# Kernel optimization log

Measured on AMD Instinct MI355X. Metric: run time of the kernel, lower is better.

## Reference

```python
import jax, jax.numpy as jnp
import numpy as np

N = 50000
EPS = 1e-12


def sage_conv(x, src, dst, Wl, bl, Wr):
    # mean aggregation of source features into target nodes
    msg = x[src]                                            # [E, d]
    agg = jax.ops.segment_sum(msg, dst, num_segments=N)     # [N, d]
    cnt = jax.ops.segment_sum(jnp.ones_like(src, dtype=x.dtype), dst, num_segments=N)
    agg = agg / jnp.maximum(cnt, 1.0)[:, None]
    out = agg @ Wl + bl + x @ Wr                            # lin_l(aggr) + lin_r(x)
    # L2 normalize (PyG normalize=True)
    nrm = jnp.maximum(jnp.linalg.norm(out, axis=-1, keepdims=True), EPS)
    return out / nrm


def setup_inputs() -> dict:
    key = jax.random.key(0)
    ks = jax.random.split(key, 12)
    d_in, d_h, d_out = 128, 128, 40
    E = 800000
    x = jax.random.normal(ks[0], (N, d_in), dtype=jnp.float32)
    edge_index = jax.random.randint(ks[1], (2, E), 0, N, dtype=jnp.int64)

    def xavier(k, shp):
        lim = np.sqrt(6.0 / (shp[0] + shp[1]))
        return jax.random.uniform(k, shp, jnp.float32, -lim, lim)

    return {
        "x": x, "edge_index": edge_index,
        "W1l": xavier(ks[2], (d_in, d_h)), "b1": jnp.zeros((d_h,), jnp.float32), "W1r": xavier(ks[3], (d_in, d_h)),
        "W2l": xavier(ks[4], (d_h, d_h)),  "b2": jnp.zeros((d_h,), jnp.float32), "W2r": xavier(ks[5], (d_h, d_h)),
        "W3l": xavier(ks[6], (d_h, d_h)),  "b3": jnp.zeros((d_h,), jnp.float32), "W3r": xavier(ks[7], (d_h, d_h)),
        "Wfc": xavier(ks[8], (d_h, d_out)), "bfc": jnp.zeros((d_out,), jnp.float32),
    }


def reference(x, edge_index, W1l, b1, W1r, W2l, b2, W2r, W3l, b3, W3r, Wfc, bfc):
    src, dst = edge_index[0], edge_index[1]
    h = sage_conv(x, src, dst, W1l, b1, W1r)
    h = jax.nn.relu(h)                       # dropout = identity at eval
    h = sage_conv(h, src, dst, W2l, b2, W2r)
    h = jax.nn.relu(h)
    h = sage_conv(h, src, dst, W3l, b3, W3r)
    return jax.nn.softmax(h @ Wfc + bfc, axis=-1)
```

## Files before the change

kernel.cpp:

```cpp
#include <hip/hip_runtime.h>
#include <math.h>

#define NN 50000
#define D 128
#define NBUK 256
#define EPB 4096

typedef __attribute__((ext_vector_type(8))) short bf16x8;
typedef __attribute__((ext_vector_type(4))) float f32x4;
typedef __attribute__((ext_vector_type(2))) float f32x2;

__device__ __forceinline__ float bf2f(unsigned short u) {
    union { unsigned int i; float f; } c;
    c.i = ((unsigned int)u) << 16;
    return c.f;
}
__device__ __forceinline__ unsigned short f2bf(float f) {
    union { float f; unsigned int i; } c;
    c.f = f;
    unsigned int u = c.i;
    return (unsigned short)((u + 0x7FFFu + ((u >> 16) & 1u)) >> 16);
}
__device__ __forceinline__ unsigned char f2f8(float v) {
    return (unsigned char)(__builtin_amdgcn_cvt_pk_fp8_f32(v, v, 0, false) & 0xFF);
}


__global__ __launch_bounds__(256) void cvtpack_kernel(const float* __restrict__ x,
                                                      unsigned short* __restrict__ xb,
                                                      unsigned int* __restrict__ x8,
                                                      int n4,
                                                      const float* __restrict__ W0,
                                                      const float* __restrict__ W1,
                                                      const float* __restrict__ W2,
                                                      const float* __restrict__ W3,
                                                      const float* __restrict__ W4,
                                                      const float* __restrict__ W5,
                                                      unsigned short* __restrict__ P,
                                                      const float* __restrict__ Wfc,
                                                      unsigned short* __restrict__ Pfc) {
    if (blockIdx.x < 384) {
        int i = blockIdx.x * 256 + threadIdx.x;
        int w = i >> 14, j = i & 16383;
        const float* W = (w == 0) ? W0 : (w == 1) ? W1 : (w == 2) ? W2
                       : (w == 3) ? W3 : (w == 4) ? W4 : W5;
        int e = j & 7, l = (j >> 3) & 63, n = (j >> 9) & 7, ks = j >> 12;
        int k = ks * 32 + (l >> 4) * 8 + e;
        int col = n * 16 + (l & 15);
        P[i] = f2bf(W[k * D + col]);
    } else if (blockIdx.x < 408) {
        int i = (blockIdx.x - 384) * 256 + threadIdx.x;
        int e = i & 7, l = (i >> 3) & 63, f = i >> 9;
        int ks = f / 3, n = f - ks * 3;
        int k = ks * 32 + (l >> 4) * 8 + e;
        int col = n * 16 + (l & 15);
        Pfc[i] = (col < 40) ? f2bf(Wfc[k * 40 + col]) : (unsigned short)0;
    } else {
        int i = (blockIdx.x - 408) * 256 + threadIdx.x;
        if (i < n4) {
            float4 v = ((const float4*)x)[i];
            ushort4 o;
            o.x = f2bf(v.x); o.y = f2bf(v.y); o.z = f2bf(v.z); o.w = f2bf(v.w);
            ((ushort4*)xb)[i] = o;
            unsigned int p01 = __builtin_amdgcn_cvt_pk_fp8_f32(v.x, v.y, 0, false);
            unsigned int p23 = __builtin_amdgcn_cvt_pk_fp8_f32(v.z, v.w, 0, false);
            x8[i] = (p01 & 0xFFFFu) | (p23 << 16);
        }
    }
}


__global__ __launch_bounds__(256) void bucket_hist_kernel(const int* __restrict__ e, int E,
                                                          int* __restrict__ bukcnt) {
    __shared__ int h[NBUK];
    int t = threadIdx.x;
    h[t] = 0;
    __syncthreads();
    int base = blockIdx.x * EPB;
    #pragma unroll
    for (int k = 0; k < 4; ++k) {
        int idx = base + k * 1024 + t * 4;
        if (idx + 4 <= E) {
            int4 d = *(const int4*)(e + E + idx);
            atomicAdd(&h[d.x >> 8], 1);
            atomicAdd(&h[d.y >> 8], 1);
            atomicAdd(&h[d.z >> 8], 1);
            atomicAdd(&h[d.w >> 8], 1);
        } else {
            for (int i = idx; i < E; ++i) atomicAdd(&h[e[E + i] >> 8], 1);
        }
    }
    __syncthreads();
    if (h[t]) atomicAdd(&bukcnt[t], h[t]);
}

__global__ __launch_bounds__(256) void bucket_scan_kernel(const int* __restrict__ bukcnt,
                                                          int* __restrict__ bukbase,
                                                          int* __restrict__ bukfill, int E) {
    __shared__ int wsum[4], woff[4];
    int t = threadIdx.x;
    int lane = t & 63, wave = t >> 6;
    int v = bukcnt[t];
    int incl = v;
    for (int off = 1; off < 64; off <<= 1) {
        int u = __shfl_up(incl, off);
        if (lane >= off) incl += u;
    }
    if (lane == 63) wsum[wave] = incl;
    __syncthreads();
    if (t == 0) {
        int r = 0;
        #pragma unroll
        for (int w = 0; w < 4; ++w) { woff[w] = r; r += wsum[w]; }
    }
    __syncthreads();
    int excl = woff[wave] + incl - v;
    bukbase[t] = excl;
    bukfill[t] = excl;
    if (t == 255) bukbase[NBUK] = E;
}

__global__ __launch_bounds__(256) void bucket_scatter_kernel(const int* __restrict__ e, int E,
                                                             int* __restrict__ bukfill,
                                                             unsigned int* __restrict__ ebuk) {
    __shared__ int h[NBUK];
    __shared__ int res[NBUK];
    int t = threadIdx.x;
    h[t] = 0;
    __syncthreads();
    int base = blockIdx.x * EPB;
    int4 d[4];
    #pragma unroll
    for (int k = 0; k < 4; ++k) {
        int idx = base + k * 1024 + t * 4;
        if (idx + 4 <= E) {
            d[k] = *(const int4*)(e + E + idx);
        } else {
            d[k].x = (idx + 0 < E) ? e[E + idx + 0] : -1;
            d[k].y = (idx + 1 < E) ? e[E + idx + 1] : -1;
            d[k].z = (idx + 2 < E) ? e[E + idx + 2] : -1;
            d[k].w = (idx + 3 < E) ? e[E + idx + 3] : -1;
        }
        if (d[k].x >= 0) atomicAdd(&h[d[k].x >> 8], 1);
        if (d[k].y >= 0) atomicAdd(&h[d[k].y >> 8], 1);
        if (d[k].z >= 0) atomicAdd(&h[d[k].z >> 8], 1);
        if (d[k].w >= 0) atomicAdd(&h[d[k].w >> 8], 1);
    }
    __syncthreads();
    res[t] = h[t] ? atomicAdd(&bukfill[t], h[t]) : 0;
    h[t] = 0;
    __syncthreads();
    #pragma unroll
    for (int k = 0; k < 4; ++k) {
        int idx = base + k * 1024 + t * 4;
        int4 s;
        if (idx + 4 <= E) {
            s = *(const int4*)(e + idx);
        } else {
            s.x = (idx + 0 < E) ? e[idx + 0] : 0;
            s.y = (idx + 1 < E) ? e[idx + 1] : 0;
            s.z = (idx + 2 < E) ? e[idx + 2] : 0;
            s.w = (idx + 3 < E) ? e[idx + 3] : 0;
        }
        if (d[k].x >= 0) { int b = d[k].x >> 8; int r = atomicAdd(&h[b], 1);
            ebuk[res[b] + r] = (unsigned int)(s.x & 0xFFFF) | ((unsigned int)(d[k].x & 255) << 16); }
        if (d[k].y >= 0) { int b = d[k].y >> 8; int r = atomicAdd(&h[b], 1);
            ebuk[res[b] + r] = (unsigned int)(s.y & 0xFFFF) | ((unsigned int)(d[k].y & 255) << 16); }
        if (d[k].z >= 0) { int b = d[k].z >> 8; int r = atomicAdd(&h[b], 1);
            ebuk[res[b] + r] = (unsigned int)(s.z & 0xFFFF) | ((unsigned int)(d[k].z & 255) << 16); }
        if (d[k].w >= 0) { int b = d[k].w >> 8; int r = atomicAdd(&h[b], 1);
            ebuk[res[b] + r] = (unsigned int)(s.w & 0xFFFF) | ((unsigned int)(d[k].w & 255) << 16); }
    }
}


__global__ __launch_bounds__(256) void cnt_scan_kernel(const unsigned int* __restrict__ ebuk,
                                                       const int* __restrict__ bukbase,
                                                       int* __restrict__ row_ptr,
                                                       float* __restrict__ inv_cnt,
                                                       int N, int E) {
    __shared__ int c[NBUK];
    __shared__ int wsum[4], woff[4];
    int t = threadIdx.x, b = blockIdx.x;
    c[t] = 0;
    __syncthreads();
    int lo = bukbase[b], hi = bukbase[b + 1];
    for (int i = lo + t; i < hi; i += 256) atomicAdd(&c[ebuk[i] >> 16], 1);
    __syncthreads();
    int v = c[t];
    int lane = t & 63, wave = t >> 6;
    int incl = v;
    for (int off = 1; off < 64; off <<= 1) {
        int u = __shfl_up(incl, off);
        if (lane >= off) incl += u;
    }
    if (lane == 63) wsum[wave] = incl;
    __syncthreads();
    if (t == 0) {
        int r = 0;
        #pragma unroll
        for (int w = 0; w < 4; ++w) { woff[w] = r; r += wsum[w]; }
    }
    __syncthreads();
    int excl = woff[wave] + incl - v;
    int g = b * NBUK + t;
    if (g < N) {
        row_ptr[g] = bukbase[b] + excl;
        inv_cnt[g] = 1.0f / fmaxf((float)v, 1.0f);
    }
    if (g == N) row_ptr[N] = E;
}

__global__ __launch_bounds__(256) void csr_scatter_kernel(const unsigned int* __restrict__ ebuk,
                                                          const int* __restrict__ bukbase,
                                                          const int* __restrict__ row_ptr,
                                                          unsigned short* __restrict__ csr_src,
                                                          int N) {
    __shared__ int rp[NBUK];
    __shared__ int lf[NBUK];
    int t = threadIdx.x, b = blockIdx.x;
    int g = b * NBUK + t;
    rp[t] = (g < N) ? row_ptr[g] : 0;
    lf[t] = 0;
    __syncthreads();
    int lo = bukbase[b], hi = bukbase[b + 1];
    for (int i = lo + t; i < hi; i += 256) {
        unsigned int v = ebuk[i];
        int dl = v >> 16;
        int r = atomicAdd(&lf[dl], 1);
        csr_src[rp[dl] + r] = (unsigned short)(v & 0xFFFF);
    }
}


__device__ __forceinline__ void acc_f8(float& x, float& y, float& z, float& w,
                                       unsigned int v) {
    f32x2 lo = __builtin_amdgcn_cvt_pk_f32_fp8(v, false);
    f32x2 hi = __builtin_amdgcn_cvt_pk_f32_fp8(v, true);
    x += lo.x; y += lo.y; z += hi.x; w += hi.y;
}

__global__ __launch_bounds__(256) void aggregate_kernel(const unsigned int* __restrict__ h8,
                                                        const int* __restrict__ row_ptr,
                                                        const unsigned short* __restrict__ csr_src,
                                                        const float* __restrict__ inv_cnt,
                                                        unsigned short* __restrict__ agg, int N) {
    int node = (int)((blockIdx.x * blockDim.x + threadIdx.x) >> 5);
    int l = threadIdx.x & 31;
    if (node >= N) return;
    int beg = row_ptr[node], end = row_ptr[node + 1];
    float a0x = 0.f, a0y = 0.f, a0z = 0.f, a0w = 0.f;
    float a1x = 0.f, a1y = 0.f, a1z = 0.f, a1w = 0.f;
    for (int base = beg; base < end; base += 32) {
        int idx = 0;
        if (base + l < end) idx = csr_src[base + l];
        int n = min(32, end - base);
        int j = 0;
        for (; j + 8 <= n; j += 8) {
            int s0 = __shfl(idx, j + 0, 32);
            int s1 = __shfl(idx, j + 1, 32);
            int s2 = __shfl(idx, j + 2, 32);
            int s3 = __shfl(idx, j + 3, 32);
            int s4 = __shfl(idx, j + 4, 32);
            int s5 = __shfl(idx, j + 5, 32);
            int s6 = __shfl(idx, j + 6, 32);
            int s7 = __shfl(idx, j + 7, 32);
            unsigned int v0 = h8[(size_t)s0 * 32 + l];
            unsigned int v1 = h8[(size_t)s1 * 32 + l];
            unsigned int v2 = h8[(size_t)s2 * 32 + l];
            unsigned int v3 = h8[(size_t)s3 * 32 + l];
            unsigned int v4 = h8[(size_t)s4 * 32 + l];
            unsigned int v5 = h8[(size_t)s5 * 32 + l];
            unsigned int v6 = h8[(size_t)s6 * 32 + l];
            unsigned int v7 = h8[(size_t)s7 * 32 + l];
            acc_f8(a0x, a0y, a0z, a0w, v0);
            acc_f8(a1x, a1y, a1z, a1w, v1);
            acc_f8(a0x, a0y, a0z, a0w, v2);
            acc_f8(a1x, a1y, a1z, a1w, v3);
            acc_f8(a0x, a0y, a0z, a0w, v4);
            acc_f8(a1x, a1y, a1z, a1w, v5);
            acc_f8(a0x, a0y, a0z, a0w, v6);
            acc_f8(a1x, a1y, a1z, a1w, v7);
        }
        for (; j < n; ++j) {
            int s = __shfl(idx, j, 32);
            acc_f8(a0x, a0y, a0z, a0w, h8[(size_t)s * 32 + l]);
        }
    }
    float iv = inv_cnt[node];
    ushort4 o;
    o.x = f2bf((a0x + a1x) * iv);
    o.y = f2bf((a0y + a1y) * iv);
    o.z = f2bf((a0z + a1z) * iv);
    o.w = f2bf((a0w + a1w) * iv);
    ((ushort4*)agg)[(size_t)node * 32 + l] = o;
}


__global__ __launch_bounds__(256) void sage_mfma_kernel(const unsigned short* __restrict__ aggb,
                                                        const unsigned short* __restrict__ xb,
                                                        const unsigned short* __restrict__ wlp,
                                                        const unsigned short* __restrict__ wrp,
                                                        const float* __restrict__ bl,
                                                        unsigned short* __restrict__ outb,
                                                        unsigned char* __restrict__ out8,
                                                        int N) {
    int t = threadIdx.x;
    int w = t >> 6;
    int l = t & 63;
    int rlo = l & 15;
    int khi = l >> 4;
    int row0 = blockIdx.x * 64 + w * 16;
    int rowA = row0 + rlo;
    bool okA = rowA < N;

    f32x4 acc[8];
    #pragma unroll
    for (int n = 0; n < 8; ++n) {
        float b = bl[n * 16 + rlo];
        acc[n] = (f32x4){b, b, b, b};
    }

    const short* Ap = (const short*)aggb + (size_t)(okA ? rowA : 0) * D + khi * 8;
    const short* Xp = (const short*)xb   + (size_t)(okA ? rowA : 0) * D + khi * 8;
    const short* WL = (const short*)wlp + l * 8;
    const short* WR = (const short*)wrp + l * 8;
    const bf16x8 Z = {0, 0, 0, 0, 0, 0, 0, 0};

    #pragma unroll 1
    for (int ks = 0; ks < 4; ++ks) {
        bf16x8 a = okA ? *(const bf16x8*)(Ap + ks * 32) : Z;
        #pragma unroll
        for (int n = 0; n < 8; ++n) {
            bf16x8 b = *(const bf16x8*)(WL + (ks * 8 + n) * 512);
            acc[n] = __builtin_amdgcn_mfma_f32_16x16x32_bf16(a, b, acc[n], 0, 0, 0);
        }
    }
    #pragma unroll 1
    for (int ks = 0; ks < 4; ++ks) {
        bf16x8 a = okA ? *(const bf16x8*)(Xp + ks * 32) : Z;
        #pragma unroll
        for (int n = 0; n < 8; ++n) {
            bf16x8 b = *(const bf16x8*)(WR + (ks * 8 + n) * 512);
            acc[n] = __builtin_amdgcn_mfma_f32_16x16x32_bf16(a, b, acc[n], 0, 0, 0);
        }
    }

    #pragma unroll
    for (int r = 0; r < 4; ++r) {
        float s = 0.f;
        #pragma unroll
        for (int n = 0; n < 8; ++n) s += acc[n][r] * acc[n][r];
        s += __shfl_xor(s, 1);
        s += __shfl_xor(s, 2);
        s += __shfl_xor(s, 4);
        s += __shfl_xor(s, 8);
        float inv = 1.0f / fmaxf(sqrtf(s), 1e-12f);
        int gr = row0 + khi * 4 + r;
        if (gr < N) {
            #pragma unroll
            for (int n = 0; n < 8; ++n) {
                float v = fmaxf(acc[n][r] * inv, 0.f);
                outb[(size_t)gr * D + n * 16 + rlo] = f2bf(v);
                out8[(size_t)gr * D + n * 16 + rlo] = f2f8(v);
            }
        }
    }
}


#define SH_STRIDE 136

__global__ __launch_bounds__(256) void sage_mfma_fc_kernel(const unsigned short* __restrict__ aggb,
                                                           const unsigned short* __restrict__ xb,
                                                           const unsigned short* __restrict__ wlp,
                                                           const unsigned short* __restrict__ wrp,
                                                           const float* __restrict__ bl,
                                                           const unsigned short* __restrict__ wfcp,
                                                           const float* __restrict__ bfc,
                                                           float* __restrict__ out, int N) {
    __shared__ unsigned short sH[64 * SH_STRIDE];
    int t = threadIdx.x;
    int w = t >> 6;
    int l = t & 63;
    int rlo = l & 15;
    int khi = l >> 4;
    int row0 = blockIdx.x * 64 + w * 16;
    int rowA = row0 + rlo;
    bool okA = rowA < N;

    f32x4 acc[8];
    #pragma unroll
    for (int n = 0; n < 8; ++n) {
        float b = bl[n * 16 + rlo];
        acc[n] = (f32x4){b, b, b, b};
    }

    const short* Ap = (const short*)aggb + (size_t)(okA ? rowA : 0) * D + khi * 8;
    const short* Xp = (const short*)xb   + (size_t)(okA ? rowA : 0) * D + khi * 8;
    const short* WL = (const short*)wlp + l * 8;
    const short* WR = (const short*)wrp + l * 8;
    const bf16x8 Z = {0, 0, 0, 0, 0, 0, 0, 0};

    #pragma unroll 1
    for (int ks = 0; ks < 4; ++ks) {
        bf16x8 a = okA ? *(const bf16x8*)(Ap + ks * 32) : Z;
        #pragma unroll
        for (int n = 0; n < 8; ++n) {
            bf16x8 b = *(const bf16x8*)(WL + (ks * 8 + n) * 512);
            acc[n] = __builtin_amdgcn_mfma_f32_16x16x32_bf16(a, b, acc[n], 0, 0, 0);
        }
    }
    #pragma unroll 1
    for (int ks = 0; ks < 4; ++ks) {
        bf16x8 a = okA ? *(const bf16x8*)(Xp + ks * 32) : Z;
        #pragma unroll
        for (int n = 0; n < 8; ++n) {
            bf16x8 b = *(const bf16x8*)(WR + (ks * 8 + n) * 512);
            acc[n] = __builtin_amdgcn_mfma_f32_16x16x32_bf16(a, b, acc[n], 0, 0, 0);
        }
    }

    #pragma unroll
    for (int r = 0; r < 4; ++r) {
        float s = 0.f;
        #pragma unroll
        for (int n = 0; n < 8; ++n) s += acc[n][r] * acc[n][r];
        s += __shfl_xor(s, 1);
        s += __shfl_xor(s, 2);
        s += __shfl_xor(s, 4);
        s += __shfl_xor(s, 8);
        float inv = 1.0f / fmaxf(sqrtf(s), 1e-12f);
        int lr = w * 16 + khi * 4 + r;
        #pragma unroll
        for (int n = 0; n < 8; ++n)
            sH[lr * SH_STRIDE + n * 16 + rlo] = f2bf(acc[n][r] * inv);
    }

    f32x4 fa[3];
    #pragma unroll
    for (int n = 0; n < 3; ++n) {
        int col = n * 16 + rlo;
        float b = (col < 40) ? bfc[col] : 0.f;
        fa[n] = (f32x4){b, b, b, b};
    }
    const short* WF = (const short*)wfcp + l * 8;
    const unsigned short* hrow = sH + (w * 16 + rlo) * SH_STRIDE + khi * 8;
    #pragma unroll
    for (int ks = 0; ks < 4; ++ks) {
        bf16x8 a = *(const bf16x8*)(hrow + ks * 32);
        #pragma unroll
        for (int n = 0; n < 3; ++n) {
            bf16x8 b = *(const bf16x8*)(WF + (ks * 3 + n) * 512);
            fa[n] = __builtin_amdgcn_mfma_f32_16x16x32_bf16(a, b, fa[n], 0, 0, 0);
        }
    }

    bool v2 = (rlo < 8);
    #pragma unroll
    for (int r = 0; r < 4; ++r) {
        float m = fmaxf(fa[0][r], fa[1][r]);
        if (v2) m = fmaxf(m, fa[2][r]);
        m = fmaxf(m, __shfl_xor(m, 1));
        m = fmaxf(m, __shfl_xor(m, 2));
        m = fmaxf(m, __shfl_xor(m, 4));
        m = fmaxf(m, __shfl_xor(m, 8));
        float e0 = expf(fa[0][r] - m);
        float e1 = expf(fa[1][r] - m);
        float e2 = v2 ? expf(fa[2][r] - m) : 0.f;
        float s = e0 + e1 + e2;
        s += __shfl_xor(s, 1);
        s += __shfl_xor(s, 2);
        s += __shfl_xor(s, 4);
        s += __shfl_xor(s, 8);
        float inv = 1.0f / s;
        int gr = row0 + khi * 4 + r;
        if (gr < N) {
            out[(size_t)gr * 40 + rlo]      = e0 * inv;
            out[(size_t)gr * 40 + 16 + rlo] = e1 * inv;
            if (v2) out[(size_t)gr * 40 + 32 + rlo] = e2 * inv;
        }
    }
}


extern "C" void kernel_launch(void* const* d_in, const int* in_sizes, int n_in,
                              void* d_out, int out_size, void* d_ws, size_t ws_size,
                              hipStream_t stream) {
    const float* x   = (const float*)d_in[0];
    const int*   e   = (const int*)d_in[1];
    const float* W1l = (const float*)d_in[2];
    const float* b1  = (const float*)d_in[3];
    const float* W1r = (const float*)d_in[4];
    const float* W2l = (const float*)d_in[5];
    const float* b2  = (const float*)d_in[6];
    const float* W2r = (const float*)d_in[7];
    const float* W3l = (const float*)d_in[8];
    const float* b3  = (const float*)d_in[9];
    const float* W3r = (const float*)d_in[10];
    const float* Wfc = (const float*)d_in[11];
    const float* bfc = (const float*)d_in[12];
    float* out = (float*)d_out;

    const int N = NN;
    const int E = in_sizes[1] / 2;

    unsigned char* p = (unsigned char*)d_ws;
    unsigned short* xb   = (unsigned short*)p; p += (size_t)N * D * 2;
    unsigned short* h1b  = (unsigned short*)p; p += (size_t)N * D * 2;
    unsigned short* h2b  = (unsigned short*)p; p += (size_t)N * D * 2;
    unsigned short* aggb = (unsigned short*)p; p += (size_t)N * D * 2;
    unsigned char*  xf8  = (unsigned char*)p;  p += (size_t)N * D;
    unsigned char*  h1f8 = (unsigned char*)p;  p += (size_t)N * D;
    unsigned short* wpk  = (unsigned short*)p; p += 6 * 16384 * 2;
    unsigned short* wfcp = (unsigned short*)p; p += 6144 * 2;
    float* inv_cnt = (float*)p; p += (size_t)N * 4;
    int* row_ptr = (int*)p; p += (size_t)(N + 4) * 4;
    int* bukcnt  = (int*)p; p += NBUK * 4;
    int* bukbase = (int*)p; p += (NBUK + 4) * 4;
    int* bukfill = (int*)p; p += NBUK * 4;
    unsigned int* ebuk = (unsigned int*)p; p += (size_t)E * 4;
    unsigned short* csr_src = (unsigned short*)p;
    unsigned char* h2f8 = xf8;

    unsigned short* w1lp = wpk;
    unsigned short* w1rp = wpk + 16384;
    unsigned short* w2lp = wpk + 2 * 16384;
    unsigned short* w2rp = wpk + 3 * 16384;
    unsigned short* w3lp = wpk + 4 * 16384;
    unsigned short* w3rp = wpk + 5 * 16384;

    hipMemsetAsync(bukcnt, 0, sizeof(int) * NBUK, stream);

    int n4 = N * D / 4;
    cvtpack_kernel<<<408 + (n4 + 255) / 256, 256, 0, stream>>>(
        x, xb, (unsigned int*)xf8, n4, W1l, W1r, W2l, W2r, W3l, W3r, wpk, Wfc, wfcp);

    int EB = (E + EPB - 1) / EPB;
    bucket_hist_kernel<<<EB, 256, 0, stream>>>(e, E, bukcnt);
    bucket_scan_kernel<<<1, 256, 0, stream>>>(bukcnt, bukbase, bukfill, E);
    bucket_scatter_kernel<<<EB, 256, 0, stream>>>(e, E, bukfill, ebuk);
    cnt_scan_kernel<<<NBUK, 256, 0, stream>>>(ebuk, bukbase, row_ptr, inv_cnt, N, E);
    csr_scatter_kernel<<<NBUK, 256, 0, stream>>>(ebuk, bukbase, row_ptr, csr_src, N);

    int aggBlocks = (N * 32 + 255) / 256;
    int sageBlocks = (N + 63) / 64;

    aggregate_kernel<<<aggBlocks, 256, 0, stream>>>((const unsigned int*)xf8, row_ptr,
                                                    csr_src, inv_cnt, aggb, N);
    sage_mfma_kernel<<<sageBlocks, 256, 0, stream>>>(aggb, xb, w1lp, w1rp, b1,
                                                     h1b, h1f8, N);

    aggregate_kernel<<<aggBlocks, 256, 0, stream>>>((const unsigned int*)h1f8, row_ptr,
                                                    csr_src, inv_cnt, aggb, N);
    sage_mfma_kernel<<<sageBlocks, 256, 0, stream>>>(aggb, h1b, w2lp, w2rp, b2,
                                                     h2b, h2f8, N);

    aggregate_kernel<<<aggBlocks, 256, 0, stream>>>((const unsigned int*)h2f8, row_ptr,
                                                    csr_src, inv_cnt, aggb, N);
    sage_mfma_fc_kernel<<<sageBlocks, 256, 0, stream>>>(aggb, h2b, w3lp, w3rp, b3,
                                                        wfcp, bfc, out, N);
}
```

Measured before the change: 172.4 us.

## Fuse neighbor aggregation into SAGE MFMA kernels and merge CSR build steps

Each layer's mean-aggregation gather now runs inside the MFMA kernel. It writes the 64 aggregated rows of a block into LDS instead of a global bf16 buffer, which removes the agg write and re-read and three kernel launches. The count-scan and CSR scatter kernels are merged into one, and the bucket-counter memset moves into the conversion kernel. The trade-off is that the gather loses its separate high-occupancy launch: 8 half-wave groups per block each handle 8 nodes before the MFMA phase can start, so latency hiding during the gather may suffer.

```diff
diff --git a/kernel.cpp b/kernel.cpp
--- a/kernel.cpp
+++ b/kernel.cpp
@@ -5,6 +5,7 @@
 #define D 128
 #define NBUK 256
 #define EPB 4096
+#define SH_STRIDE 136
 
 typedef __attribute__((ext_vector_type(8))) short bf16x8;
 typedef __attribute__((ext_vector_type(4))) float f32x4;
@@ -38,7 +39,8 @@
                                                       const float* __restrict__ W5,
                                                       unsigned short* __restrict__ P,
                                                       const float* __restrict__ Wfc,
-                                                      unsigned short* __restrict__ Pfc) {
+                                                      unsigned short* __restrict__ Pfc,
+                                                      int* __restrict__ bukcnt) {
     if (blockIdx.x < 384) {
         int i = blockIdx.x * 256 + threadIdx.x;
         int w = i >> 14, j = i & 16383;
@@ -49,6 +51,7 @@
         int col = n * 16 + (l & 15);
         P[i] = f2bf(W[k * D + col]);
     } else if (blockIdx.x < 408) {
+        if (blockIdx.x == 384) bukcnt[threadIdx.x] = 0;
         int i = (blockIdx.x - 384) * 256 + threadIdx.x;
         int e = i & 7, l = (i >> 3) & 63, f = i >> 9;
         int ks = f / 3, n = f - ks * 3;
@@ -174,12 +177,14 @@
 }
 
 
-__global__ __launch_bounds__(256) void cnt_scan_kernel(const unsigned int* __restrict__ ebuk,
-                                                       const int* __restrict__ bukbase,
-                                                       int* __restrict__ row_ptr,
-                                                       float* __restrict__ inv_cnt,
-                                                       int N, int E) {
+__global__ __launch_bounds__(256) void cnt_scan_scatter_kernel(const unsigned int* __restrict__ ebuk,
+                                                               const int* __restrict__ bukbase,
+                                                               int* __restrict__ row_ptr,
+                                                               float* __restrict__ inv_cnt,
+                                                               unsigned short* __restrict__ csr_src,
+                                                               int N, int E) {
     __shared__ int c[NBUK];
+    __shared__ int rp[NBUK];
     __shared__ int wsum[4], woff[4];
     int t = threadIdx.x, b = blockIdx.x;
     c[t] = 0;
@@ -203,32 +208,20 @@
     }
     __syncthreads();
     int excl = woff[wave] + incl - v;
+    rp[t] = bukbase[b] + excl;
+    c[t] = 0;
     int g = b * NBUK + t;
     if (g < N) {
-        row_ptr[g] = bukbase[b] + excl;
+        row_ptr[g] = rp[t];
         inv_cnt[g] = 1.0f / fmaxf((float)v, 1.0f);
     }
     if (g == N) row_ptr[N] = E;
-}
-
-__global__ __launch_bounds__(256) void csr_scatter_kernel(const unsigned int* __restrict__ ebuk,
-                                                          const int* __restrict__ bukbase,
-                                                          const int* __restrict__ row_ptr,
-                                                          unsigned short* __restrict__ csr_src,
-                                                          int N) {
-    __shared__ int rp[NBUK];
-    __shared__ int lf[NBUK];
-    int t = threadIdx.x, b = blockIdx.x;
-    int g = b * NBUK + t;
-    rp[t] = (g < N) ? row_ptr[g] : 0;
-    lf[t] = 0;
-    __syncthreads();
-    int lo = bukbase[b], hi = bukbase[b + 1];
+    __syncthreads();
     for (int i = lo + t; i < hi; i += 256) {
-        unsigned int v = ebuk[i];
-        int dl = v >> 16;
-        int r = atomicAdd(&lf[dl], 1);
-        csr_src[rp[dl] + r] = (unsigned short)(v & 0xFFFF);
+        unsigned int u = ebuk[i];
+        int dl = u >> 16;
+        int r = atomicAdd(&c[dl], 1);
+        csr_src[rp[dl] + r] = (unsigned short)(u & 0xFFFF);
     }
 }
 
@@ -240,78 +233,90 @@
     x += lo.x; y += lo.y; z += hi.x; w += hi.y;
 }
 
-__global__ __launch_bounds__(256) void aggregate_kernel(const unsigned int* __restrict__ h8,
-                                                        const int* __restrict__ row_ptr,
-                                                        const unsigned short* __restrict__ csr_src,
-                                                        const float* __restrict__ inv_cnt,
-                                                        unsigned short* __restrict__ agg, int N) {
-    int node = (int)((blockIdx.x * blockDim.x + threadIdx.x) >> 5);
-    int l = threadIdx.x & 31;
-    if (node >= N) return;
-    int beg = row_ptr[node], end = row_ptr[node + 1];
-    float a0x = 0.f, a0y = 0.f, a0z = 0.f, a0w = 0.f;
-    float a1x = 0.f, a1y = 0.f, a1z = 0.f, a1w = 0.f;
-    for (int base = beg; base < end; base += 32) {
-        int idx = 0;
-        if (base + l < end) idx = csr_src[base + l];
-        int n = min(32, end - base);
-        int j = 0;
-        for (; j + 8 <= n; j += 8) {
-            int s0 = __shfl(idx, j + 0, 32);
-            int s1 = __shfl(idx, j + 1, 32);
-            int s2 = __shfl(idx, j + 2, 32);
-            int s3 = __shfl(idx, j + 3, 32);
-            int s4 = __shfl(idx, j + 4, 32);
-            int s5 = __shfl(idx, j + 5, 32);
-            int s6 = __shfl(idx, j + 6, 32);
-            int s7 = __shfl(idx, j + 7, 32);
-            unsigned int v0 = h8[(size_t)s0 * 32 + l];
-            unsigned int v1 = h8[(size_t)s1 * 32 + l];
-            unsigned int v2 = h8[(size_t)s2 * 32 + l];
-            unsigned int v3 = h8[(size_t)s3 * 32 + l];
-            unsigned int v4 = h8[(size_t)s4 * 32 + l];
-            unsigned int v5 = h8[(size_t)s5 * 32 + l];
-            unsigned int v6 = h8[(size_t)s6 * 32 + l];
-            unsigned int v7 = h8[(size_t)s7 * 32 + l];
-            acc_f8(a0x, a0y, a0z, a0w, v0);
-            acc_f8(a1x, a1y, a1z, a1w, v1);
-            acc_f8(a0x, a0y, a0z, a0w, v2);
-            acc_f8(a1x, a1y, a1z, a1w, v3);
-            acc_f8(a0x, a0y, a0z, a0w, v4);
-            acc_f8(a1x, a1y, a1z, a1w, v5);
-            acc_f8(a0x, a0y, a0z, a0w, v6);
-            acc_f8(a1x, a1y, a1z, a1w, v7);
-        }
-        for (; j < n; ++j) {
-            int s = __shfl(idx, j, 32);
-            acc_f8(a0x, a0y, a0z, a0w, h8[(size_t)s * 32 + l]);
-        }
-    }
-    float iv = inv_cnt[node];
-    ushort4 o;
-    o.x = f2bf((a0x + a1x) * iv);
-    o.y = f2bf((a0y + a1y) * iv);
-    o.z = f2bf((a0z + a1z) * iv);
-    o.w = f2bf((a0w + a1w) * iv);
-    ((ushort4*)agg)[(size_t)node * 32 + l] = o;
-}
-
-
-__global__ __launch_bounds__(256) void sage_mfma_kernel(const unsigned short* __restrict__ aggb,
-                                                        const unsigned short* __restrict__ xb,
-                                                        const unsigned short* __restrict__ wlp,
-                                                        const unsigned short* __restrict__ wrp,
-                                                        const float* __restrict__ bl,
-                                                        unsigned short* __restrict__ outb,
-                                                        unsigned char* __restrict__ out8,
-                                                        int N) {
+__device__ __forceinline__ void gather_rows_to_lds(const unsigned int* __restrict__ h8,
+                                                   const int* __restrict__ row_ptr,
+                                                   const unsigned short* __restrict__ csr_src,
+                                                   const float* __restrict__ inv_cnt,
+                                                   unsigned short* __restrict__ sA,
+                                                   int row0, int t, int N) {
+    int g32 = t >> 5, l = t & 31;
+    for (int ni = g32; ni < 64; ni += 8) {
+        int node = row0 + ni;
+        ushort4 o = make_ushort4(0, 0, 0, 0);
+        if (node < N) {
+            int beg = row_ptr[node], end = row_ptr[node + 1];
+            float a0x = 0.f, a0y = 0.f, a0z = 0.f, a0w = 0.f;
+            float a1x = 0.f, a1y = 0.f, a1z = 0.f, a1w = 0.f;
+            for (int base = beg; base < end; base += 32) {
+                int idx = 0;
+                if (base + l < end) idx = csr_src[base + l];
+                int n = min(32, end - base);
+                int j = 0;
+                for (; j + 8 <= n; j += 8) {
+                    int s0 = __shfl(idx, j + 0, 32);
+                    int s1 = __shfl(idx, j + 1, 32);
+                    int s2 = __shfl(idx, j + 2, 32);
+                    int s3 = __shfl(idx, j + 3, 32);
+                    int s4 = __shfl(idx, j + 4, 32);
+                    int s5 = __shfl(idx, j + 5, 32);
+                    int s6 = __shfl(idx, j + 6, 32);
+                    int s7 = __shfl(idx, j + 7, 32);
+                    unsigned int v0 = h8[(size_t)s0 * 32 + l];
+                    unsigned int v1 = h8[(size_t)s1 * 32 + l];
+                    unsigned int v2 = h8[(size_t)s2 * 32 + l];
+                    unsigned int v3 = h8[(size_t)s3 * 32 + l];
+                    unsigned int v4 = h8[(size_t)s4 * 32 + l];
+                    unsigned int v5 = h8[(size_t)s5 * 32 + l];
+                    unsigned int v6 = h8[(size_t)s6 * 32 + l];
+                    unsigned int v7 = h8[(size_t)s7 * 32 + l];
+                    acc_f8(a0x, a0y, a0z, a0w, v0);
+                    acc_f8(a1x, a1y, a1z, a1w, v1);
+                    acc_f8(a0x, a0y, a0z, a0w, v2);
+                    acc_f8(a1x, a1y, a1z, a1w, v3);
+                    acc_f8(a0x, a0y, a0z, a0w, v4);
+                    acc_f8(a1x, a1y, a1z, a1w, v5);
+                    acc_f8(a0x, a0y, a0z, a0w, v6);
+                    acc_f8(a1x, a1y, a1z, a1w, v7);
+                }
+                for (; j < n; ++j) {
+                    int s = __shfl(idx, j, 32);
+                    acc_f8(a0x, a0y, a0z, a0w, h8[(size_t)s * 32 + l]);
+                }
+            }
+            float iv = inv_cnt[node];
+            o.x = f2bf((a0x + a1x) * iv);
+            o.y = f2bf((a0y + a1y) * iv);
+            o.z = f2bf((a0z + a1z) * iv);
+            o.w = f2bf((a0w + a1w) * iv);
+        }
+        *(ushort4*)(sA + ni * SH_STRIDE + l * 4) = o;
+    }
+}
+
+__global__ __launch_bounds__(256) void sage_fused_kernel(const unsigned int* __restrict__ h8,
+                                                         const unsigned short* __restrict__ xb,
+                                                         const int* __restrict__ row_ptr,
+                                                         const unsigned short* __restrict__ csr_src,
+                                                         const float* __restrict__ inv_cnt,
+                                                         const unsigned short* __restrict__ wlp,
+                                                         const unsigned short* __restrict__ wrp,
+                                                         const float* __restrict__ bl,
+                                                         unsigned short* __restrict__ outb,
+                                                         unsigned char* __restrict__ out8,
+                                                         int N) {
+    __shared__ unsigned short sA[64 * SH_STRIDE];
     int t = threadIdx.x;
+    int row0 = blockIdx.x * 64;
+
+    gather_rows_to_lds(h8, row_ptr, csr_src, inv_cnt, sA, row0, t, N);
+    __syncthreads();
+
     int w = t >> 6;
     int l = t & 63;
     int rlo = l & 15;
     int khi = l >> 4;
-    int row0 = blockIdx.x * 64 + w * 16;
-    int rowA = row0 + rlo;
+    int wrow0 = row0 + w * 16;
+    int rowA = wrow0 + rlo;
     bool okA = rowA < N;
 
     f32x4 acc[8];
@@ -321,15 +326,15 @@
         acc[n] = (f32x4){b, b, b, b};
     }
 
-    const short* Ap = (const short*)aggb + (size_t)(okA ? rowA : 0) * D + khi * 8;
-    const short* Xp = (const short*)xb   + (size_t)(okA ? rowA : 0) * D + khi * 8;
+    const unsigned short* Ar = sA + (w * 16 + rlo) * SH_STRIDE + khi * 8;
+    const short* Xp = (const short*)xb + (size_t)(okA ? rowA : 0) * D + khi * 8;
     const short* WL = (const short*)wlp + l * 8;
     const short* WR = (const short*)wrp + l * 8;
     const bf16x8 Z = {0, 0, 0, 0, 0, 0, 0, 0};
 
     #pragma unroll 1
     for (int ks = 0; ks < 4; ++ks) {
-        bf16x8 a = okA ? *(const bf16x8*)(Ap + ks * 32) : Z;
+        bf16x8 a = *(const bf16x8*)(Ar + ks * 32);
         #pragma unroll
         for (int n = 0; n < 8; ++n) {
             bf16x8 b = *(const bf16x8*)(WL + (ks * 8 + n) * 512);
@@ -356,7 +361,7 @@
         s += __shfl_xor(s, 4);
         s += __shfl_xor(s, 8);
         float inv = 1.0f / fmaxf(sqrtf(s), 1e-12f);
-        int gr = row0 + khi * 4 + r;
+        int gr = wrow0 + khi * 4 + r;
         if (gr < N) {
             #pragma unroll
             for (int n = 0; n < 8; ++n) {
@@ -369,24 +374,30 @@
 }
 
 
-#define SH_STRIDE 136
-
-__global__ __launch_bounds__(256) void sage_mfma_fc_kernel(const unsigned short* __restrict__ aggb,
-                                                           const unsigned short* __restrict__ xb,
-                                                           const unsigned short* __restrict__ wlp,
-                                                           const unsigned short* __restrict__ wrp,
-                                                           const float* __restrict__ bl,
-                                                           const unsigned short* __restrict__ wfcp,
-                                                           const float* __restrict__ bfc,
-                                                           float* __restrict__ out, int N) {
-    __shared__ unsigned short sH[64 * SH_STRIDE];
+__global__ __launch_bounds__(256) void sage_fused_fc_kernel(const unsigned int* __restrict__ h8,
+                                                            const unsigned short* __restrict__ xb,
+                                                            const int* __restrict__ row_ptr,
+                                                            const unsigned short* __restrict__ csr_src,
+                                                            const float* __restrict__ inv_cnt,
+                                                            const unsigned short* __restrict__ wlp,
+                                                            const unsigned short* __restrict__ wrp,
+                                                            const float* __restrict__ bl,
+                                                            const unsigned short* __restrict__ wfcp,
+                                                            const float* __restrict__ bfc,
+                                                            float* __restrict__ out, int N) {
+    __shared__ unsigned short sA[64 * SH_STRIDE];
     int t = threadIdx.x;
+    int row0 = blockIdx.x * 64;
+
+    gather_rows_to_lds(h8, row_ptr, csr_src, inv_cnt, sA, row0, t, N);
+    __syncthreads();
+
     int w = t >> 6;
     int l = t & 63;
     int rlo = l & 15;
     int khi = l >> 4;
-    int row0 = blockIdx.x * 64 + w * 16;
-    int rowA = row0 + rlo;
+    int wrow0 = row0 + w * 16;
+    int rowA = wrow0 + rlo;
     bool okA = rowA < N;
 
     f32x4 acc[8];
@@ -396,15 +407,15 @@
         acc[n] = (f32x4){b, b, b, b};
     }
 
-    const short* Ap = (const short*)aggb + (size_t)(okA ? rowA : 0) * D + khi * 8;
-    const short* Xp = (const short*)xb   + (size_t)(okA ? rowA : 0) * D + khi * 8;
+    const unsigned short* Ar = sA + (w * 16 + rlo) * SH_STRIDE + khi * 8;
+    const short* Xp = (const short*)xb + (size_t)(okA ? rowA : 0) * D + khi * 8;
     const short* WL = (const short*)wlp + l * 8;
     const short* WR = (const short*)wrp + l * 8;
     const bf16x8 Z = {0, 0, 0, 0, 0, 0, 0, 0};
 
     #pragma unroll 1
     for (int ks = 0; ks < 4; ++ks) {
-        bf16x8 a = okA ? *(const bf16x8*)(Ap + ks * 32) : Z;
+        bf16x8 a = *(const bf16x8*)(Ar + ks * 32);
         #pragma unroll
         for (int n = 0; n < 8; ++n) {
             bf16x8 b = *(const bf16x8*)(WL + (ks * 8 + n) * 512);
@@ -434,7 +445,7 @@
         int lr = w * 16 + khi * 4 + r;
         #pragma unroll
         for (int n = 0; n < 8; ++n)
-            sH[lr * SH_STRIDE + n * 16 + rlo] = f2bf(acc[n][r] * inv);
+            sA[lr * SH_STRIDE + n * 16 + rlo] = f2bf(acc[n][r] * inv);
     }
 
     f32x4 fa[3];
@@ -445,7 +456,7 @@
         fa[n] = (f32x4){b, b, b, b};
     }
     const short* WF = (const short*)wfcp + l * 8;
-    const unsigned short* hrow = sH + (w * 16 + rlo) * SH_STRIDE + khi * 8;
+    const unsigned short* hrow = sA + (w * 16 + rlo) * SH_STRIDE + khi * 8;
     #pragma unroll
     for (int ks = 0; ks < 4; ++ks) {
         bf16x8 a = *(const bf16x8*)(hrow + ks * 32);
@@ -474,7 +485,7 @@
         s += __shfl_xor(s, 4);
         s += __shfl_xor(s, 8);
         float inv = 1.0f / s;
-        int gr = row0 + khi * 4 + r;
+        int gr = wrow0 + khi * 4 + r;
         if (gr < N) {
             out[(size_t)gr * 40 + rlo]      = e0 * inv;
             out[(size_t)gr * 40 + 16 + rlo] = e1 * inv;
@@ -509,7 +520,6 @@
     unsigned short* xb   = (unsigned short*)p; p += (size_t)N * D * 2;
     unsigned short* h1b  = (unsigned short*)p; p += (size_t)N * D * 2;
     unsigned short* h2b  = (unsigned short*)p; p += (size_t)N * D * 2;
-    unsigned short* aggb = (unsigned short*)p; p += (size_t)N * D * 2;
     unsigned char*  xf8  = (unsigned char*)p;  p += (size_t)N * D;
     unsigned char*  h1f8 = (unsigned char*)p;  p += (size_t)N * D;
     unsigned short* wpk  = (unsigned short*)p; p += 6 * 16384 * 2;
@@ -530,34 +540,29 @@
     unsigned short* w3lp = wpk + 4 * 16384;
     unsigned short* w3rp = wpk + 5 * 16384;
 
-    hipMemsetAsync(bukcnt, 0, sizeof(int) * NBUK, stream);
-
     int n4 = N * D / 4;
     cvtpack_kernel<<<408 + (n4 + 255) / 256, 256, 0, stream>>>(
-        x, xb, (unsigned int*)xf8, n4, W1l, W1r, W2l, W2r, W3l, W3r, wpk, Wfc, wfcp);
+        x, xb, (unsigned int*)xf8, n4, W1l, W1r, W2l, W2r, W3l, W3r, wpk,
+        Wfc, wfcp, bukcnt);
 
     int EB = (E + EPB - 1) / EPB;
     bucket_hist_kernel<<<EB, 256, 0, stream>>>(e, E, bukcnt);
     bucket_scan_kernel<<<1, 256, 0, stream>>>(bukcnt, bukbase, bukfill, E);
     bucket_scatter_kernel<<<EB, 256, 0, stream>>>(e, E, bukfill, ebuk);
-    cnt_scan_kernel<<<NBUK, 256, 0, stream>>>(ebuk, bukbase, row_ptr, inv_cnt, N, E);
-    csr_scatter_kernel<<<NBUK, 256, 0, stream>>>(ebuk, bukbase, row_ptr, csr_src, N);
-
-    int aggBlocks = (N * 32 + 255) / 256;
+    cnt_scan_scatter_kernel<<<NBUK, 256, 0, stream>>>(ebuk, bukbase, row_ptr,
+                                                      inv_cnt, csr_src, N, E);
+
     int sageBlocks = (N + 63) / 64;
 
-    aggregate_kernel<<<aggBlocks, 256, 0, stream>>>((const unsigned int*)xf8, row_ptr,
-                                                    csr_src, inv_cnt, aggb, N);
-    sage_mfma_kernel<<<sageBlocks, 256, 0, stream>>>(aggb, xb, w1lp, w1rp, b1,
-                                                     h1b, h1f8, N);
-
-    aggregate_kernel<<<aggBlocks, 256, 0, stream>>>((const unsigned int*)h1f8, row_ptr,
-                                                    csr_src, inv_cnt, aggb, N);
-    sage_mfma_kernel<<<sageBlocks, 256, 0, stream>>>(aggb, h1b, w2lp, w2rp, b2,
-                                                     h2b, h2f8, N);
-
-    aggregate_kernel<<<aggBlocks, 256, 0, stream>>>((const unsigned int*)h2f8, row_ptr,
-                                                    csr_src, inv_cnt, aggb, N);
-    sage_mfma_fc_kernel<<<sageBlocks, 256, 0, stream>>>(aggb, h2b, w3lp, w3rp, b3,
-                                                        wfcp, bfc, out, N);
-}
+    sage_fused_kernel<<<sageBlocks, 256, 0, stream>>>(
+        (const unsigned int*)xf8, xb, row_ptr, csr_src, inv_cnt,
+        w1lp, w1rp, b1, h1b, h1f8, N);
+
+    sage_fused_kernel<<<sageBlocks, 256, 0, stream>>>(
+        (const unsigned int*)h1f8, h1b, row_ptr, csr_src, inv_cnt,
+        w2lp, w2rp, b2, h2b, h2f8, N);
+
+    sage_fused_fc_kernel<<<sageBlocks, 256, 0, stream>>>(
+        (const unsigned int*)h2f8, h2b, row_ptr, csr_src, inv_cnt,
+        w3lp, w3rp, b3, wfcp, bfc, out, N);
+}
```

Measured after the change: 186.2 us. +8.0%, slower.
